# Optimization experiments

Measured on AMD Instinct MI355X. Metric: run time of the kernel, lower is better.

The kernel has to match this reference:

```python
import jax, jax.numpy as jnp
import numpy as np

EPS = 1e-12  # torch F.normalize eps


def _l2norm(x):
    # L2 normalize along last dim, matching torch.nn.functional.normalize
    n = jnp.sqrt(jnp.sum(x * x, axis=-1, keepdims=True))
    return x / jnp.maximum(n, EPS)


def setup_inputs() -> dict:
    key = jax.random.key(0)
    ks = jax.random.split(key, 7)
    B, Lq, Ld, H, D = 128, 32, 512, 768, 128
    return {
        "q_hidden": jax.random.normal(ks[0], (B, Lq, H), dtype=jnp.float32),
        "pd_hidden": jax.random.normal(ks[1], (B, Ld, H), dtype=jnp.float32),
        "nd_hidden": jax.random.normal(ks[2], (B, Ld, H), dtype=jnp.float32),
        "W": jax.random.normal(ks[3], (H, D), dtype=jnp.float32) * 0.02,
        "b": jax.random.normal(ks[4], (D,), dtype=jnp.float32) * 0.02,
        "pd_mask": jax.random.randint(ks[5], (B, Ld), 0, 2, dtype=jnp.int32),
        "nd_mask": jax.random.randint(ks[6], (B, Ld), 0, 2, dtype=jnp.int32),
    }


def reference(q_hidden, pd_hidden, nd_hidden, W, b, pd_mask, nd_mask):
    # query embedding: linear projection then L2 normalize
    Q = _l2norm(q_hidden @ W + b)                       # [B, Lq, D]
    # doc embedding: project, zero out punctuation/pad tokens, normalize
    PD = _l2norm((pd_hidden @ W + b) * pd_mask[..., None].astype(q_hidden.dtype))
    ND = _l2norm((nd_hidden @ W + b) * nd_mask[..., None].astype(q_hidden.dtype))
    # late-interaction MaxSim: max over doc tokens, sum over query tokens
    pos = jnp.einsum("bqd,bkd->bqk", Q, PD).max(axis=2).sum(axis=1)  # [B]
    neg = jnp.einsum("bqd,bkd->bqk", Q, ND).max(axis=2).sum(axis=1)  # [B]
    return jnp.stack([pos, neg], axis=-1)               # [B, 2]
```

## Files before the change

kernel.cpp:

```cpp
#include <hip/hip_runtime.h>
#include <hip/hip_bf16.h>

typedef short v8s __attribute__((ext_vector_type(8)));
typedef float v4f __attribute__((ext_vector_type(4)));

#define MFMA16(a, b, c) __builtin_amdgcn_mfma_f32_16x16x32_bf16((a), (b), (c), 0, 0, 0)

typedef __attribute__((address_space(1))) const void g_void;
typedef __attribute__((address_space(3))) void lds_void;
#define GLOAD_LDS16(g, l) \
    __builtin_amdgcn_global_load_lds((g_void*)(g), (lds_void*)(l), 16, 0, 0)

constexpr int Bsz   = 128;
constexpr int Lq    = 32;
constexpr int Ld    = 512;
constexpr int H     = 768;
constexpr int D     = 128;
constexpr int QROWS = Bsz * Lq;
constexpr int DROWS = Bsz * Ld;
constexpr int MTOT  = QROWS + 2 * DROWS;
constexpr int BM    = 64;
constexpr int BK    = 64;
constexpr int NT    = H / BK;
static_assert(QROWS % BM == 0 && DROWS % BM == 0, "block never spans sources");

static __device__ __forceinline__ unsigned short f2b(float f) {
    unsigned int u = __builtin_bit_cast(unsigned int, f);
    unsigned int r = u + 0x7FFFu + ((u >> 16) & 1u);
    return (unsigned short)(r >> 16);
}
static __device__ __forceinline__ unsigned int pack2(float a, float b) {
    return (unsigned int)f2b(a) | ((unsigned int)f2b(b) << 16);
}

__global__ void prep_w_kernel(const float* __restrict__ W,
                              unsigned short* __restrict__ Wt) {
    int idx = blockIdx.x * 256 + threadIdx.x;
    if (idx < H * D) {
        int d = idx / H, h = idx % H;
        Wt[idx] = f2b(W[h * D + d]);
    }
}

__global__ __launch_bounds__(256, 4) void proj_norm_kernel(
    const float* __restrict__ qh, const float* __restrict__ pdh,
    const float* __restrict__ ndh, const float* __restrict__ bias,
    const int* __restrict__ pdm, const int* __restrict__ ndm,
    const unsigned short* __restrict__ Wt, unsigned short* __restrict__ emb)
{
    __shared__ unsigned short Abuf[2][BM * BK];
    __shared__ unsigned short Wbuf[2][D * BK];
    __shared__ float ssred[2][BM];

    const int tid  = threadIdx.x;
    const int lane = tid & 63, wave = tid >> 6;
    const int l15  = lane & 15, lg = lane >> 4;
    const int mg   = wave >> 1;
    const int ng   = wave & 1;
    const long row0 = (long)blockIdx.x * BM;

    const float* src; const int* mask; long srow;
    if (row0 < QROWS)              { src = qh;  srow = row0;                 mask = nullptr; }
    else if (row0 < QROWS + DROWS) { src = pdh; srow = row0 - QROWS;         mask = pdm; }
    else                           { src = ndh; srow = row0 - QROWS - DROWS; mask = ndm; }

    const int rr = tid >> 2;
    const int cc = tid & 3;
    const float* gA = src + (srow + rr) * (long)H + cc * 16;

    float4 rA[4];

    auto issueA = [&](int kt) {
#pragma unroll
        for (int j = 0; j < 4; ++j)
            rA[j] = *(const float4*)(gA + kt * BK + j * 4);
    };
    auto writeA = [&](int bi) {
#pragma unroll
        for (int j = 0; j < 4; ++j) {
            const int sl = (cc * 4 + j) ^ ((rr & 7) << 1);
            uint2 u;
            u.x = pack2(rA[j].x, rA[j].y);
            u.y = pack2(rA[j].z, rA[j].w);
            *(uint2*)(&Abuf[bi][rr * 64 + sl * 4]) = u;
        }
    };

    auto stageW = [&](int bi, int kt) {
#pragma unroll
        for (int i = 0; i < 4; ++i) {
            const int d  = 32 * wave + 8 * i + (lane >> 3);
            const int cw = (lane & 7) ^ (lane >> 3);
            const unsigned short* gp = Wt + (size_t)d * H + kt * BK + cw * 8;
            GLOAD_LDS16(gp, &Wbuf[bi][(32 * wave + 8 * i) * BK]);
        }
    };

    v4f acc[2][4];
#pragma unroll
    for (int mt = 0; mt < 2; ++mt)
#pragma unroll
        for (int nt = 0; nt < 4; ++nt) acc[mt][nt] = (v4f){0.f, 0.f, 0.f, 0.f};

    auto compute = [&](int bi) {
#pragma unroll
        for (int kk = 0; kk < 2; ++kk) {
            v8s wfr[4];
#pragma unroll
            for (int nt = 0; nt < 4; ++nt) {
                const int d  = ng * 64 + nt * 16 + l15;
                const int ch = (kk * 4 + lg) ^ (l15 & 7);
                wfr[nt] = *(const v8s*)(&Wbuf[bi][d * BK + ch * 8]);
            }
#pragma unroll
            for (int mt = 0; mt < 2; ++mt) {
                const int r  = mg * 32 + mt * 16 + l15;
                const int ch = (kk * 4 + lg) ^ (r & 7);
                v8s a = *(const v8s*)(&Abuf[bi][r * 64 + ch * 8]);
#pragma unroll
                for (int nt = 0; nt < 4; ++nt)
                    acc[mt][nt] = MFMA16(a, wfr[nt], acc[mt][nt]);
            }
        }
    };

    issueA(0); stageW(0, 0);
    asm volatile("s_waitcnt vmcnt(4)" ::: "memory");
    writeA(0);
    issueA(1); stageW(1, 1);
    asm volatile("s_waitcnt vmcnt(8)" ::: "memory");
    asm volatile("s_waitcnt lgkmcnt(0)" ::: "memory");
    __builtin_amdgcn_sched_barrier(0);
    __builtin_amdgcn_s_barrier();

#pragma unroll
    for (int t = 0; t < NT; ++t) {
        compute(t & 1);
        if (t + 1 < NT) {
            __builtin_amdgcn_sched_barrier(0);
            asm volatile("s_waitcnt vmcnt(4)" ::: "memory");
            writeA((t + 1) & 1);
            if (t + 2 < NT) {
                issueA(t + 2);
                stageW(t & 1 , t + 2);
                asm volatile("s_waitcnt vmcnt(8)" ::: "memory");
            } else {
                asm volatile("s_waitcnt vmcnt(0)" ::: "memory");
            }
            asm volatile("s_waitcnt lgkmcnt(0)" ::: "memory");
            __builtin_amdgcn_sched_barrier(0);
            __builtin_amdgcn_s_barrier();
        }
    }

    float bv[4];
#pragma unroll
    for (int nt = 0; nt < 4; ++nt) bv[nt] = bias[ng * 64 + nt * 16 + l15];

    float ss[2][4];
#pragma unroll
    for (int mt = 0; mt < 2; ++mt)
#pragma unroll
        for (int q = 0; q < 4; ++q) {
            float s = 0.f;
#pragma unroll
            for (int nt = 0; nt < 4; ++nt) {
                float v = acc[mt][nt][q] + bv[nt];
                acc[mt][nt][q] = v;
                s += v * v;
            }
            ss[mt][q] = s;
        }
#pragma unroll
    for (int off = 1; off < 16; off <<= 1)
#pragma unroll
        for (int mt = 0; mt < 2; ++mt)
#pragma unroll
            for (int q = 0; q < 4; ++q)
                ss[mt][q] += __shfl_xor(ss[mt][q], off);

    if (l15 == 0) {
#pragma unroll
        for (int mt = 0; mt < 2; ++mt)
#pragma unroll
            for (int q = 0; q < 4; ++q)
                ssred[ng][mg * 32 + mt * 16 + lg * 4 + q] = ss[mt][q];
    }
    __syncthreads();

#pragma unroll
    for (int mt = 0; mt < 2; ++mt)
#pragma unroll
        for (int q = 0; q < 4; ++q) {
            const int row = mg * 32 + mt * 16 + lg * 4 + q;
            float t = ssred[0][row] + ssred[1][row];
            float s = 1.0f / fmaxf(sqrtf(t), 1e-12f);
            if (mask) s *= (float)mask[srow + row];
            unsigned short* op = emb + (size_t)(row0 + row) * D + ng * 64 + l15;
#pragma unroll
            for (int nt = 0; nt < 4; ++nt)
                op[nt * 16] = f2b(acc[mt][nt][q] * s);
        }
}

__global__ __launch_bounds__(256) void maxsim_kernel(
    const unsigned short* __restrict__ emb, float* __restrict__ out)
{
    const int blk  = blockIdx.x;
    const int b    = blk >> 1, side = blk & 1;
    const int wave = threadIdx.x >> 6, lane = threadIdx.x & 63;
    const int l15  = lane & 15, lg = lane >> 4;

    const unsigned short* Q  = emb + (size_t)(b * Lq) * D;
    const unsigned short* Dm = emb + (size_t)(QROWS + side * DROWS + b * Ld) * D;

    v4f acc[2][8];
#pragma unroll
    for (int m = 0; m < 2; ++m)
#pragma unroll
        for (int n = 0; n < 8; ++n) acc[m][n] = (v4f){0.f, 0.f, 0.f, 0.f};

    const int tok0 = wave * 128;
#pragma unroll
    for (int kk = 0; kk < 4; ++kk) {
        const int k0 = kk * 32 + lg * 8;
        v8s qa0 = *(const v8s*)(Q + (size_t)(l15) * D + k0);
        v8s qa1 = *(const v8s*)(Q + (size_t)(16 + l15) * D + k0);
#pragma unroll
        for (int n = 0; n < 8; ++n) {
            v8s db = *(const v8s*)(Dm + (size_t)(tok0 + n * 16 + l15) * D + k0);
            acc[0][n] = MFMA16(qa0, db, acc[0][n]);
            acc[1][n] = MFMA16(qa1, db, acc[1][n]);
        }
    }

    float mx[2][4];
#pragma unroll
    for (int m = 0; m < 2; ++m)
#pragma unroll
        for (int r = 0; r < 4; ++r) {
            float v = acc[m][0][r];
#pragma unroll
            for (int n = 1; n < 8; ++n) v = fmaxf(v, acc[m][n][r]);
            mx[m][r] = v;
        }
#pragma unroll
    for (int off = 1; off < 16; off <<= 1) {
#pragma unroll
        for (int m = 0; m < 2; ++m)
#pragma unroll
            for (int r = 0; r < 4; ++r)
                mx[m][r] = fmaxf(mx[m][r], __shfl_xor(mx[m][r], off));
    }

    __shared__ float red[4][32];
    if (l15 == 0) {
#pragma unroll
        for (int m = 0; m < 2; ++m)
#pragma unroll
            for (int r = 0; r < 4; ++r)
                red[wave][m * 16 + lg * 4 + r] = mx[m][r];
    }
    __syncthreads();

    if (threadIdx.x < 32) {
        int q = threadIdx.x;
        float v = fmaxf(fmaxf(red[0][q], red[1][q]), fmaxf(red[2][q], red[3][q]));
#pragma unroll
        for (int off = 1; off < 32; off <<= 1) v += __shfl_xor(v, off);
        if (q == 0) out[blk] = v;
    }
}

extern "C" void kernel_launch(void* const* d_in, const int* in_sizes, int n_in,
                              void* d_out, int out_size, void* d_ws, size_t ws_size,
                              hipStream_t stream)
{
    const float* qh   = (const float*)d_in[0];
    const float* pdh  = (const float*)d_in[1];
    const float* ndh  = (const float*)d_in[2];
    const float* W    = (const float*)d_in[3];
    const float* bias = (const float*)d_in[4];
    const int*   pdm  = (const int*)d_in[5];
    const int*   ndm  = (const int*)d_in[6];
    float* out = (float*)d_out;

    unsigned short* Wt  = (unsigned short*)d_ws;
    unsigned short* emb = Wt + (size_t)H * D;

    prep_w_kernel<<<(H * D + 255) / 256, 256, 0, stream>>>(W, Wt);
    proj_norm_kernel<<<MTOT / BM, 256, 0, stream>>>(qh, pdh, ndh, bias, pdm, ndm, Wt, emb);
    maxsim_kernel<<<Bsz * 2, 256, 0, stream>>>(emb, out);
}
```

Measured before the change: 130.7 us.

## Compact masked doc tokens and skip projecting and scoring zeroed rows

Adds a compaction kernel that builds per-batch lists of unmasked document token indices and their counts. The projection kernel then gathers only the unmasked rows, and blocks past the count exit early. MaxSim iterates over the compacted tokens only, seeding the max with 0 whenever some tokens are masked, since masked rows normalise to zero vectors. This roughly halves the projection GEMM work and memory traffic for random masks, at the cost of gathered row loads and an extra kernel launch.

Result: faster. 105.2 us (-19.5%).

```diff
diff --git a/kernel.cpp b/kernel.cpp
--- a/kernel.cpp
+++ b/kernel.cpp
@@ -18,11 +18,11 @@
 constexpr int D     = 128;
 constexpr int QROWS = Bsz * Lq;
 constexpr int DROWS = Bsz * Ld;
-constexpr int MTOT  = QROWS + 2 * DROWS;
 constexpr int BM    = 64;
 constexpr int BK    = 64;
 constexpr int NT    = H / BK;
-static_assert(QROWS % BM == 0 && DROWS % BM == 0, "block never spans sources");
+constexpr int NQB   = QROWS / BM;
+constexpr int NDG   = (Ld / BM) * Bsz;
 
 static __device__ __forceinline__ unsigned short f2b(float f) {
     unsigned int u = __builtin_bit_cast(unsigned int, f);
@@ -42,31 +42,76 @@
     }
 }
 
+__global__ __launch_bounds__(64) void compact_kernel(
+    const int* __restrict__ pdm, const int* __restrict__ ndm,
+    int* __restrict__ idx, int* __restrict__ cnt)
+{
+    const int blk  = blockIdx.x;
+    const int side = blk >> 7, b = blk & 127;
+    const int lane = threadIdx.x;
+    const int* m = (side ? ndm : pdm) + b * Ld;
+    int* op = idx + (size_t)blk * Ld;
+
+    int off = 0;
+#pragma unroll
+    for (int c = 0; c < Ld / 64; ++c) {
+        const int t = c * 64 + lane;
+        const bool p = (m[t] != 0);
+        unsigned long long bal = __ballot(p);
+        int pre = __popcll(bal & ((1ull << lane) - 1ull));
+        if (p) op[off + pre] = t;
+        off += __popcll(bal);
+    }
+    if (lane == 0) cnt[blk] = off;
+}
+
 __global__ __launch_bounds__(256, 4) void proj_norm_kernel(
     const float* __restrict__ qh, const float* __restrict__ pdh,
     const float* __restrict__ ndh, const float* __restrict__ bias,
-    const int* __restrict__ pdm, const int* __restrict__ ndm,
+    const int* __restrict__ idx, const int* __restrict__ cnt,
     const unsigned short* __restrict__ Wt, unsigned short* __restrict__ emb)
 {
     __shared__ unsigned short Abuf[2][BM * BK];
     __shared__ unsigned short Wbuf[2][D * BK];
     __shared__ float ssred[2][BM];
+    __shared__ int   ridx[BM];
+    __shared__ int   eidx[BM];
 
     const int tid  = threadIdx.x;
     const int lane = tid & 63, wave = tid >> 6;
     const int l15  = lane & 15, lg = lane >> 4;
     const int mg   = wave >> 1;
     const int ng   = wave & 1;
-    const long row0 = (long)blockIdx.x * BM;
-
-    const float* src; const int* mask; long srow;
-    if (row0 < QROWS)              { src = qh;  srow = row0;                 mask = nullptr; }
-    else if (row0 < QROWS + DROWS) { src = pdh; srow = row0 - QROWS;         mask = pdm; }
-    else                           { src = ndh; srow = row0 - QROWS - DROWS; mask = ndm; }
+    const int bid  = blockIdx.x;
+
+    const float* src;
+    if (bid < NQB) {
+        src = qh;
+        if (tid < BM) {
+            ridx[tid] = bid * BM + tid;
+            eidx[tid] = bid * BM + tid;
+        }
+    } else {
+        const int t    = bid - NQB;
+        const int side = t >> 10;
+        const int g    = t & (NDG - 1);
+        const int b    = g >> 3, lgr = g & 7;
+        const int c    = cnt[side * 128 + b];
+        if (lgr * BM >= c) return;
+        src = side ? ndh : pdh;
+        if (tid < BM) {
+            int jj = lgr * BM + tid;
+            if (jj >= c) jj = c - 1;
+            const int tok = idx[(size_t)(side * 128 + b) * Ld + jj];
+            ridx[tid] = b * Ld + tok;
+            eidx[tid] = QROWS + side * DROWS + b * Ld + tok;
+        }
+    }
+    __syncthreads();
 
     const int rr = tid >> 2;
     const int cc = tid & 3;
-    const float* gA = src + (srow + rr) * (long)H + cc * 16;
+    const float* gA = src + (size_t)ridx[rr] * H + cc * 16;
 
     float4 rA[4];
 
@@ -195,8 +240,7 @@
             const int row = mg * 32 + mt * 16 + lg * 4 + q;
             float t = ssred[0][row] + ssred[1][row];
             float s = 1.0f / fmaxf(sqrtf(t), 1e-12f);
-            if (mask) s *= (float)mask[srow + row];
-            unsigned short* op = emb + (size_t)(row0 + row) * D + ng * 64 + l15;
+            unsigned short* op = emb + (size_t)eidx[row] * D + ng * 64 + l15;
 #pragma unroll
             for (int nt = 0; nt < 4; ++nt)
                 op[nt * 16] = f2b(acc[mt][nt][q] * s);
@@ -204,67 +248,76 @@
 }
 
 __global__ __launch_bounds__(256) void maxsim_kernel(
-    const unsigned short* __restrict__ emb, float* __restrict__ out)
+    const unsigned short* __restrict__ emb,
+    const int* __restrict__ idx, const int* __restrict__ cnt,
+    float* __restrict__ out)
 {
     const int blk  = blockIdx.x;
     const int b    = blk >> 1, side = blk & 1;
     const int wave = threadIdx.x >> 6, lane = threadIdx.x & 63;
     const int l15  = lane & 15, lg = lane >> 4;
 
+    const int c = cnt[side * 128 + b];
+    const int* idxp = idx + (size_t)(side * 128 + b) * Ld;
+
     const unsigned short* Q  = emb + (size_t)(b * Lq) * D;
-    const unsigned short* Dm = emb + (size_t)(QROWS + side * DROWS + b * Ld) * D;
-
-    v4f acc[2][8];
+    const unsigned short* Dbase = emb + (size_t)(QROWS + side * DROWS + b * Ld) * D;
+
+    v8s qa[2][4];
 #pragma unroll
     for (int m = 0; m < 2; ++m)
 #pragma unroll
-        for (int n = 0; n < 8; ++n) acc[m][n] = (v4f){0.f, 0.f, 0.f, 0.f};
-
-    const int tok0 = wave * 128;
-#pragma unroll
-    for (int kk = 0; kk < 4; ++kk) {
-        const int k0 = kk * 32 + lg * 8;
-        v8s qa0 = *(const v8s*)(Q + (size_t)(l15) * D + k0);
-        v8s qa1 = *(const v8s*)(Q + (size_t)(16 + l15) * D + k0);
-#pragma unroll
-        for (int n = 0; n < 8; ++n) {
-            v8s db = *(const v8s*)(Dm + (size_t)(tok0 + n * 16 + l15) * D + k0);
-            acc[0][n] = MFMA16(qa0, db, acc[0][n]);
-            acc[1][n] = MFMA16(qa1, db, acc[1][n]);
-        }
-    }
-
+        for (int kk = 0; kk < 4; ++kk)
+            qa[m][kk] = *(const v8s*)(Q + (size_t)(m * 16 + l15) * D + kk * 32 + lg * 8);
+
+    const float minit = (c < Ld) ? 0.0f : -3.0e38f;
     float mx[2][4];
 #pragma unroll
     for (int m = 0; m < 2; ++m)
 #pragma unroll
-        for (int r = 0; r < 4; ++r) {
-            float v = acc[m][0][r];
-#pragma unroll
-            for (int n = 1; n < 8; ++n) v = fmaxf(v, acc[m][n][r]);
-            mx[m][r] = v;
-        }
-#pragma unroll
-    for (int off = 1; off < 16; off <<= 1) {
+        for (int q = 0; q < 4; ++q) mx[m][q] = minit;
+
+    for (int j0 = wave * 16; j0 < c; j0 += 64) {
+        int jj = j0 + l15;
+        if (jj >= c) jj = c - 1;
+        const int tok = idxp[jj];
+        const unsigned short* dp = Dbase + (size_t)tok * D + lg * 8;
+        v8s db0 = *(const v8s*)(dp);
+        v8s db1 = *(const v8s*)(dp + 32);
+        v8s db2 = *(const v8s*)(dp + 64);
+        v8s db3 = *(const v8s*)(dp + 96);
+#pragma unroll
+        for (int m = 0; m < 2; ++m) {
+            v4f a = (v4f){0.f, 0.f, 0.f, 0.f};
+            a = MFMA16(qa[m][0], db0, a);
+            a = MFMA16(qa[m][1], db1, a);
+            a = MFMA16(qa[m][2], db2, a);
+            a = MFMA16(qa[m][3], db3, a);
+#pragma unroll
+            for (int q = 0; q < 4; ++q) mx[m][q] = fmaxf(mx[m][q], a[q]);
+        }
+    }
+
+#pragma unroll
+    for (int off = 1; off < 16; off <<= 1)
 #pragma unroll
         for (int m = 0; m < 2; ++m)
 #pragma unroll
-            for (int r = 0; r < 4; ++r)
-                mx[m][r] = fmaxf(mx[m][r], __shfl_xor(mx[m][r], off));
-    }
+            for (int q = 0; q < 4; ++q)
+                mx[m][q] = fmaxf(mx[m][q], __shfl_xor(mx[m][q], off));
 
     __shared__ float red[4][32];
     if (l15 == 0) {
 #pragma unroll
         for (int m = 0; m < 2; ++m)
 #pragma unroll
-            for (int r = 0; r < 4; ++r)
-                red[wave][m * 16 + lg * 4 + r] = mx[m][r];
+            for (int q = 0; q < 4; ++q)
+                red[wave][m * 16 + lg * 4 + q] = mx[m][q];
     }
     __syncthreads();
 
     if (threadIdx.x < 32) {
-        int q = threadIdx.x;
+        const int q = threadIdx.x;
         float v = fmaxf(fmaxf(red[0][q], red[1][q]), fmaxf(red[2][q], red[3][q]));
 #pragma unroll
         for (int off = 1; off < 32; off <<= 1) v += __shfl_xor(v, off);
@@ -285,10 +338,15 @@
     const int*   ndm  = (const int*)d_in[6];
     float* out = (float*)d_out;
 
-    unsigned short* Wt  = (unsigned short*)d_ws;
-    unsigned short* emb = Wt + (size_t)H * D;
+    char* wsb = (char*)d_ws;
+    unsigned short* Wt  = (unsigned short*)wsb;
+    int*            idx = (int*)(wsb + 196608);
+    int*            cnt = (int*)(wsb + 196608 + 524288);
+    unsigned short* emb = (unsigned short*)(wsb + 196608 + 524288 + 1024);
 
     prep_w_kernel<<<(H * D + 255) / 256, 256, 0, stream>>>(W, Wt);
-    proj_norm_kernel<<<MTOT / BM, 256, 0, stream>>>(qh, pdh, ndh, bias, pdm, ndm, Wt, emb);
-    maxsim_kernel<<<Bsz * 2, 256, 0, stream>>>(emb, out);
-}
+    compact_kernel<<<256, 64, 0, stream>>>(pdm, ndm, idx, cnt);
+    proj_norm_kernel<<<NQB + 2 * NDG, 256, 0, stream>>>(qh, pdh, ndh, bias,
+                                                        idx, cnt, Wt, emb);
+    maxsim_kernel<<<Bsz * 2, 256, 0, stream>>>(emb, idx, cnt, out);
+}
```
